# Performance work log

Measured on AMD Instinct MI355X. Metric: run time of the kernel, lower is better.

## Reference

```python
import jax, jax.numpy as jnp
import numpy as np

IN_F = 3072       # in_features
OUT_F = 9216      # out_features = 3 * N_HEADS * HEAD_DIM (fused QKV)
GROUP = 64        # quantization group size
RANK = 32         # lora_rank
HEAD_DIM = 128
N_HEADS = OUT_F // (3 * HEAD_DIM)  # 24
EPS = 1e-6
LORA_SCALE = 1.0


def setup_inputs() -> dict:
    key = jax.random.key(0)
    ks = jax.random.split(key, 10)
    B, S = 1, 4096
    x = jax.random.normal(ks[0], (B, S, IN_F), dtype=jnp.float32)
    # packed int4 weights: two signed int4 values per int8 byte
    qweight = jax.random.randint(ks[1], (OUT_F, IN_F // 2), -128, 128, dtype=jnp.int32).astype(jnp.int8)
    wscales = (jax.random.uniform(ks[2], (IN_F // GROUP, OUT_F)) * 0.02 + 0.001).astype(jnp.float32)
    bias = (jax.random.normal(ks[3], (OUT_F,)) * 0.01).astype(jnp.float32)
    lora_down = (jax.random.normal(ks[4], (IN_F, RANK)) * 0.02).astype(jnp.float32)
    lora_up = (jax.random.normal(ks[5], (OUT_F, RANK)) * 0.02).astype(jnp.float32)
    smooth = (jax.random.uniform(ks[6], (IN_F,)) * 0.5 + 0.75).astype(jnp.float32)   # keep away from 0
    norm_q = (jax.random.uniform(ks[7], (HEAD_DIM,)) * 0.5 + 0.75).astype(jnp.float32)
    norm_k = (jax.random.uniform(ks[8], (HEAD_DIM,)) * 0.5 + 0.75).astype(jnp.float32)
    ang = jax.random.uniform(ks[9], (S, HEAD_DIM // 2)) * (2.0 * np.pi)
    rotary_emb = jnp.stack([jnp.cos(ang), jnp.sin(ang)], axis=-1).astype(jnp.float32)  # [S, D/2, 2]
    return dict(x=x, qweight=qweight, wscales=wscales, bias=bias, lora_down=lora_down,
                lora_up=lora_up, smooth=smooth, norm_q=norm_q, norm_k=norm_k, rotary_emb=rotary_emb)


def _dequant_weight(qweight, wscales):
    # unpack two signed int4 lanes from each int8 (low nibble first), then per-group scale
    low = jnp.right_shift(jnp.left_shift(qweight, 4), 4)   # arithmetic shifts on int8 -> sign extend
    high = jnp.right_shift(qweight, 4)
    w4 = jnp.stack([low, high], axis=-1).reshape(OUT_F, IN_F)          # int4 codes in [-8, 7]
    wg = w4.astype(jnp.float32).reshape(OUT_F, IN_F // GROUP, GROUP)
    return (wg * wscales.T[:, :, None]).reshape(OUT_F, IN_F)          # [N, K]


def _quantize_act(x, smooth, lora_down):
    # fused: smooth -> symmetric per-token per-group int4 quantize -> lora_down projection
    B, S, K = x.shape
    M = B * S
    xs = (x / smooth).reshape(M, K)
    xg = xs.reshape(M, K // GROUP, GROUP)
    ascale = jnp.max(jnp.abs(xg), axis=-1, keepdims=True) / 7.0
    ascale = jnp.maximum(ascale, 1e-8)
    q = jnp.clip(jnp.round(xg / ascale), -8.0, 7.0)
    deq = (q * ascale).reshape(M, K)                                   # dequantized int4 activation
    lora_act = xs @ lora_down                                          # [M, RANK], fp32 side path
    return deq, lora_act


def _rope(t, cos, sin):
    # interleaved pairs (even, odd) rotation; t: [M, H, D], cos/sin: [M, 1, D/2]
    e, o = t[..., 0::2], t[..., 1::2]
    re = e * cos - o * sin
    ro = e * sin + o * cos
    return jnp.stack([re, ro], axis=-1).reshape(t.shape)


def reference(x, qweight, wscales, bias, lora_down, lora_up, smooth, norm_q, norm_k, rotary_emb):
    B, S, K = x.shape
    M = B * S
    deq_x, lora_act = _quantize_act(x, smooth, lora_down)
    w = _dequant_weight(qweight, wscales)
    # main int4 GEMM + LoRA up + bias, all fused in the real kernel
    out = deq_x @ w.T + (LORA_SCALE * lora_act) @ lora_up.T + bias     # [M, OUT_F]
    qkv = out.reshape(M, 3, N_HEADS, HEAD_DIM)
    q, k, v = qkv[:, 0], qkv[:, 1], qkv[:, 2]
    def rms(t, g):
        return t * jax.lax.rsqrt(jnp.mean(t * t, axis=-1, keepdims=True) + EPS) * g
    q = rms(q, norm_q)
    k = rms(k, norm_k)
    cos = rotary_emb[:, None, :, 0]   # [M, 1, D/2]
    sin = rotary_emb[:, None, :, 1]
    q = _rope(q, cos, sin)
    k = _rope(k, cos, sin)
    return jnp.stack([q, k, v], axis=1).reshape(B, S, OUT_F)
```

## Files before the change

kernel.cpp:

```cpp
#include <hip/hip_runtime.h>
#include <cstdint>

#define MDIM 4096
#define NDIM 9216
#define KDIM 3072
#define KP   3136
#define NKT2 97

#define QROWS 4
#define QB2 1024
#define WB 13824
#define PB 2304

typedef unsigned int u32;
typedef unsigned short u16;
typedef float f32x4 __attribute__((ext_vector_type(4)));
typedef __bf16 bf16x8 __attribute__((ext_vector_type(8)));

__device__ __forceinline__ u16 f2bf(float f) {
  u32 u = __float_as_uint(f);
  u32 r = u + 0x7fffu + ((u >> 16) & 1u);
  return (u16)(r >> 16);
}

__device__ __forceinline__ float frcp(float f) { return __builtin_amdgcn_rcpf(f); }

__device__ __forceinline__ void gld_lds16(const void* g, void* l) {
  __builtin_amdgcn_global_load_lds((__attribute__((address_space(1))) void*)g,
                                   (__attribute__((address_space(3))) void*)l,
                                   16, 0, 0);
}

__global__ __launch_bounds__(256) void k_quant(const float* __restrict__ x,
                        const float* __restrict__ lora_down, const float* __restrict__ smooth,
                        u16* __restrict__ Aex) {
  __shared__ float xs_s[QROWS][KDIM];
  __shared__ float part[64 * 32];
  const int tid = threadIdx.x;
  const int m0 = blockIdx.x * QROWS;
  const int sub = tid & 15;

  #pragma unroll
  for (int r = 0; r < QROWS; ++r) {
    const float* xr = x + (size_t)(m0 + r) * KDIM;
    u16* arow = Aex + (size_t)(m0 + r) * KP;
    #pragma unroll
    for (int p = 0; p < 3; ++p) {
      int g = p * 16 + (tid >> 4);
      int k0 = g * 64 + sub * 4;
      float4 xv = *(const float4*)(xr + k0);
      float4 sv = *(const float4*)(smooth + k0);
      float a0 = xv.x * frcp(sv.x), a1 = xv.y * frcp(sv.y);
      float a2 = xv.z * frcp(sv.z), a3 = xv.w * frcp(sv.w);
      xs_s[r][k0+0] = a0; xs_s[r][k0+1] = a1; xs_s[r][k0+2] = a2; xs_s[r][k0+3] = a3;
      float am = fmaxf(fmaxf(fabsf(a0), fabsf(a1)), fmaxf(fabsf(a2), fabsf(a3)));
      am = fmaxf(am, __shfl_xor(am, 8, 16));
      am = fmaxf(am, __shfl_xor(am, 4, 16));
      am = fmaxf(am, __shfl_xor(am, 2, 16));
      am = fmaxf(am, __shfl_xor(am, 1, 16));
      float asc = fmaxf(am * (1.0f / 7.0f), 1e-8f);
      float iasc = frcp(asc);
      float q0 = fminf(7.f, fmaxf(-8.f, rintf(a0 * iasc)));
      float q1 = fminf(7.f, fmaxf(-8.f, rintf(a1 * iasc)));
      float q2 = fminf(7.f, fmaxf(-8.f, rintf(a2 * iasc)));
      float q3 = fminf(7.f, fmaxf(-8.f, rintf(a3 * iasc)));
      float d0 = q0 * asc, d1 = q1 * asc, d2 = q2 * asc, d3 = q3 * asc;
      u32 lo = (u32)f2bf(d0) | ((u32)f2bf(d1) << 16);
      u32 hi = (u32)f2bf(d2) | ((u32)f2bf(d3) << 16);
      *(uint2*)(arow + k0) = make_uint2(lo, hi);
    }
    if (tid < 32) arow[3104 + tid] = 0;
  }
  __syncthreads();

  const int c  = tid >> 2;
  const int r8 = (tid & 3) * 8;
  float a[QROWS][8] = {};
  const float* lp = lora_down + (size_t)c * 32 + r8;
  #pragma unroll 2
  for (int i = 0; i < 48; ++i) {
    float4 l0 = *(const float4*)(lp);
    float4 l1 = *(const float4*)(lp + 4);
    #pragma unroll
    for (int r = 0; r < QROWS; ++r) {
      float xv = xs_s[r][i * 64 + c];
      a[r][0] = fmaf(xv, l0.x, a[r][0]); a[r][1] = fmaf(xv, l0.y, a[r][1]);
      a[r][2] = fmaf(xv, l0.z, a[r][2]); a[r][3] = fmaf(xv, l0.w, a[r][3]);
      a[r][4] = fmaf(xv, l1.x, a[r][4]); a[r][5] = fmaf(xv, l1.y, a[r][5]);
      a[r][6] = fmaf(xv, l1.z, a[r][6]); a[r][7] = fmaf(xv, l1.w, a[r][7]);
    }
    lp += 64 * 32;
  }
  #pragma unroll 1
  for (int r = 0; r < QROWS; ++r) {
    __syncthreads();
    *(float4*)(&part[c * 32 + r8])     = make_float4(a[r][0], a[r][1], a[r][2], a[r][3]);
    *(float4*)(&part[c * 32 + r8 + 4]) = make_float4(a[r][4], a[r][5], a[r][6], a[r][7]);
    __syncthreads();
    if (tid < 32) {
      float s = 0.f;
      #pragma unroll 8
      for (int cc = 0; cc < 64; ++cc) s += part[cc * 32 + tid];
      Aex[(size_t)(m0 + r) * KP + 3072 + tid] = f2bf(s);
    }
  }
}

__global__ __launch_bounds__(256) void k_wdq(const u32* __restrict__ qw,
                        const float* __restrict__ wsc, const float* __restrict__ lora_up,
                        u16* __restrict__ Bex) {
  const int tid = threadIdx.x;
  int bid = blockIdx.x;

  if (bid >= WB) {
    int idx = (bid - WB) * 256 + tid;
    int n = idx >> 6, c = idx & 63;
    u16 v = 0;
    if (c < 32) v = f2bf(lora_up[n * 32 + c]);
    Bex[(size_t)n * KP + 3072 + c] = v;
    return;
  }
  __shared__ int s_viol;
  u32 probe = qw[tid];
  bool ok = (probe >> 8) == ((probe & 0x80u) ? 0xffffffu : 0u);
  if (tid == 0) s_viol = 0;
  __syncthreads();
  if (!ok) atomicOr(&s_viol, 1);
  __syncthreads();
  const int f = (s_viol == 0);

  int idx = bid * 256 + tid;
  int n = idx / 384;
  int j = idx - n * 384;
  int k0 = j * 8;
  u32 w;
  if (f) {
    uint4 q4 = ((const uint4*)qw)[idx];
    w = (q4.x & 0xffu) | ((q4.y & 0xffu) << 8) | ((q4.z & 0xffu) << 16) | ((q4.w & 0xffu) << 24);
  } else {
    w = qw[idx];
  }
  float ws = wsc[(k0 >> 6) * NDIM + n];
  u32 ow[4];
  #pragma unroll
  for (int b = 0; b < 4; ++b) {
    int by = (int)((w >> (8 * b)) & 0xffu);
    int lo = (by << 28) >> 28;
    int hi = (by << 24) >> 28;
    ow[b] = (u32)f2bf((float)lo * ws) | ((u32)f2bf((float)hi * ws) << 16);
  }
  *(uint4*)(Bex + (size_t)n * KP + k0) = make_uint4(ow[0], ow[1], ow[2], ow[3]);
}

__global__ __launch_bounds__(512) void k_gemm(const u16* __restrict__ A, const u16* __restrict__ B,
                                              const float* __restrict__ bias, const float* __restrict__ norm_q,
                                              const float* __restrict__ norm_k, const float* __restrict__ rot,
                                              float* __restrict__ out) {
  extern __shared__ u16 lds[];
  const int tid  = threadIdx.x;
  const int lane = tid & 63;
  const int wave = tid >> 6;
  const int m0 = blockIdx.y * 256;
  const int n0 = blockIdx.x * 256;
  const int wm = (wave >> 2) * 128;
  const int wn = (wave & 3) * 64;
  const int lr = lane & 15;
  const int lq = lane >> 4;

  const u16 *pA0, *pA1, *pB0, *pB1;
  int la0, la1, lb0, lb1;
  {
    auto mk = [&](int p, const u16* base, int nb) -> const u16* {
      int pr = p >> 3, cs = p & 7;
      int c  = cs ^ (pr & 7);
      int r  = pr * 2 + (c >> 2);
      int kc = c & 3;
      return base + (size_t)(nb + r) * KP + kc * 8;
    };
    int p0 = tid, p1 = 512 + tid;
    pA0 = mk(p0, A, m0); pA1 = mk(p1, A, m0);
    pB0 = mk(p0, B, n0); pB1 = mk(p1, B, n0);
    la0 = p0 * 8;        la1 = p1 * 8;
    lb0 = 8192 + p0 * 8; lb1 = 8192 + p1 * 8;
  }

  int aoff[8], boff[4];
  #pragma unroll
  for (int t = 0; t < 8; ++t) {
    int ra = wm + t * 16 + lr;
    int pr = ra >> 1, c = (ra & 1) * 4 + lq;
    aoff[t] = pr * 64 + ((c ^ (pr & 7)) * 8);
  }
  #pragma unroll
  for (int t = 0; t < 4; ++t) {
    int rb = wn + t * 16 + lr;
    int pr = rb >> 1, c = (rb & 1) * 4 + lq;
    boff[t] = 8192 + pr * 64 + ((c ^ (pr & 7)) * 8);
  }

  f32x4 acc[8][4] = {};

  #pragma unroll
  for (int s = 0; s < 3; ++s) {
    u16* sl = lds + (s << 14);
    gld_lds16(pA0, sl + la0); gld_lds16(pA1, sl + la1);
    gld_lds16(pB0, sl + lb0); gld_lds16(pB1, sl + lb1);
    pA0 += 32; pA1 += 32; pB0 += 32; pB1 += 32;
  }
  asm volatile("s_waitcnt vmcnt(4)" ::: "memory");
  __builtin_amdgcn_s_barrier();
  asm volatile("" ::: "memory");

  bf16x8 af[8], bf[4];
  #pragma unroll
  for (int t = 0; t < 8; ++t) af[t] = *(const bf16x8*)&lds[aoff[t]];
  #pragma unroll
  for (int t = 0; t < 4; ++t) bf[t] = *(const bf16x8*)&lds[boff[t]];

  #pragma unroll 1
  for (int kt = 0; kt < NKT2 - 1; ++kt) {
    u16* stl = lds + (((kt + 3) & 3) << 14);
    const u16* nsl = lds + (((kt + 1) & 3) << 14);
    if (kt < NKT2 - 3) {
      gld_lds16(pA0, stl + la0); gld_lds16(pA1, stl + la1);
      gld_lds16(pB0, stl + lb0); gld_lds16(pB1, stl + lb1);
      pA0 += 32; pA1 += 32; pB0 += 32; pB1 += 32;
    }
    __builtin_amdgcn_s_setprio(1);
    #pragma unroll
    for (int t = 0; t < 8; ++t) {
      #pragma unroll
      for (int tj = 0; tj < 4; ++tj)
        acc[t][tj] = __builtin_amdgcn_mfma_f32_16x16x32_bf16(af[t], bf[tj], acc[t][tj], 0, 0, 0);
      af[t] = *(const bf16x8*)&nsl[aoff[t]];
    }
    #pragma unroll
    for (int t = 0; t < 4; ++t) bf[t] = *(const bf16x8*)&nsl[boff[t]];
    __builtin_amdgcn_s_setprio(0);
    __builtin_amdgcn_sched_group_barrier(0x020, 4, 0);
    #pragma unroll
    for (int g = 0; g < 8; ++g) {
      __builtin_amdgcn_sched_group_barrier(0x008, 4, 0);
      __builtin_amdgcn_sched_group_barrier(0x100, 1, 0);
    }
    __builtin_amdgcn_sched_group_barrier(0x100, 4, 0);
    if (kt < NKT2 - 3) asm volatile("s_waitcnt vmcnt(4)" ::: "memory");
    else               asm volatile("s_waitcnt vmcnt(0)" ::: "memory");
    __builtin_amdgcn_s_barrier();
    asm volatile("" ::: "memory");
  }
  #pragma unroll
  for (int t = 0; t < 8; ++t)
    #pragma unroll
    for (int tj = 0; tj < 4; ++tj)
      acc[t][tj] = __builtin_amdgcn_mfma_f32_16x16x32_bf16(af[t], bf[tj], acc[t][tj], 0, 0, 0);

  const int sel = (blockIdx.x >= 24) ? 2 : (blockIdx.x >= 12 ? 1 : 0);

  float bv[4];
  #pragma unroll
  for (int tj = 0; tj < 4; ++tj) bv[tj] = bias[n0 + wn + tj * 16 + lr];
  #pragma unroll
  for (int ti = 0; ti < 8; ++ti)
    #pragma unroll
    for (int tj = 0; tj < 4; ++tj)
      #pragma unroll
      for (int rg = 0; rg < 4; ++rg)
        acc[ti][tj][rg] += bv[tj];

  if (sel == 2) {
    #pragma unroll
    for (int tj = 0; tj < 4; ++tj) {
      int n = n0 + wn + tj * 16 + lr;
      #pragma unroll
      for (int ti = 0; ti < 8; ++ti) {
        int mr = m0 + wm + ti * 16 + lq * 4;
        #pragma unroll
        for (int rg = 0; rg < 4; ++rg)
          out[(size_t)(mr + rg) * NDIM + n] = acc[ti][tj][rg];
      }
    }
    return;
  }

  __syncthreads();
  float* ssq = (float*)lds;
  #pragma unroll
  for (int ti = 0; ti < 8; ++ti) {
    float pr4[4];
    #pragma unroll
    for (int rg = 0; rg < 4; ++rg) {
      float s = 0.f;
      #pragma unroll
      for (int tj = 0; tj < 4; ++tj) s += acc[ti][tj][rg] * acc[ti][tj][rg];
      pr4[rg] = s;
    }
    #pragma unroll
    for (int off = 1; off < 16; off <<= 1)
      #pragma unroll
      for (int rg = 0; rg < 4; ++rg) pr4[rg] += __shfl_xor(pr4[rg], off);
    #pragma unroll
    for (int rg = 0; rg < 4; ++rg)
      if (lr == (ti & 3) * 4 + rg)
        ssq[(wn >> 6) * 256 + wm + ti * 16 + lq * 4 + rg] = pr4[rg];
  }
  __syncthreads();

  const float* nrm = sel ? norm_k : norm_q;
  float gm[4];
  #pragma unroll
  for (int tj = 0; tj < 4; ++tj) gm[tj] = nrm[(wn & 64) + tj * 16 + lr];
  const float2* rot2 = (const float2*)rot;
  const float sgn = (lr & 1) ? 1.0f : -1.0f;
  const int hb = (wn >> 7) * 512;

  #pragma unroll
  for (int ti = 0; ti < 8; ++ti) {
    #pragma unroll
    for (int rg = 0; rg < 4; ++rg) {
      int row = wm + ti * 16 + lq * 4 + rg;
      float tot = ssq[hb + row] + ssq[hb + 256 + row];
      float rs = rsqrtf(tot * (1.0f / 128.0f) + 1e-6f);
      int m = m0 + row;
      #pragma unroll
      for (int tj = 0; tj < 4; ++tj) {
        int nl = (wn & 64) + tj * 16 + lr;
        float v = acc[ti][tj][rg] * rs * gm[tj];
        float p = __shfl_xor(v, 1);
        float2 cs = rot2[(size_t)m * 64 + (nl >> 1)];
        out[(size_t)m * NDIM + n0 + wn + tj * 16 + lr] = v * cs.x + sgn * (p * cs.y);
      }
    }
  }
}

extern "C" void kernel_launch(void* const* d_in, const int* in_sizes, int n_in,
                              void* d_out, int out_size, void* d_ws, size_t ws_size,
                              hipStream_t stream) {
  const float* x         = (const float*)d_in[0];
  const u32*   qweight   = (const u32*)d_in[1];
  const float* wscales   = (const float*)d_in[2];
  const float* bias      = (const float*)d_in[3];
  const float* lora_down = (const float*)d_in[4];
  const float* lora_up   = (const float*)d_in[5];
  const float* smooth    = (const float*)d_in[6];
  const float* norm_q    = (const float*)d_in[7];
  const float* norm_k    = (const float*)d_in[8];
  const float* rot       = (const float*)d_in[9];
  float* out = (float*)d_out;

  u16* Aex = (u16*)d_ws;
  u16* Bex = Aex + (size_t)MDIM * KP;

  static bool attr_set = false;
  if (!attr_set) {
    hipFuncSetAttribute(reinterpret_cast<const void*>(k_gemm),
                        hipFuncAttributeMaxDynamicSharedMemorySize, 131072);
    attr_set = true;
  }

  k_wdq<<<WB + PB, 256, 0, stream>>>(qweight, wscales, lora_up, Bex);
  k_quant<<<QB2, 256, 0, stream>>>(x, lora_down, smooth, Aex);
  k_gemm<<<dim3(NDIM / 256, MDIM / 256), 512, 131072, stream>>>(Aex, Bex, bias, norm_q, norm_k, rot, out);
}
```

Measured before the change: 513.0 us.

## Use 4 waves with 128x128 warp tiles and in-register RMSNorm reduction

The GEMM block shrinks from 8 waves to 4, each computing a 128x128 sub-tile (8x8 MFMA tiles) instead of 128x64. This raises per-wave register reuse of A/B fragments, halves LDS fragment reads per MFMA, and lets each wave hold a full head dimension so the RMSNorm reduction is done with lane shuffles, without the LDS round trip and two barriers. The trade-off is doubled accumulator registers (256 VGPRs of acc), fewer waves to hide latency, and a reworked MFMA/LDS interleave schedule without setprio.

```diff
diff --git a/kernel.cpp b/kernel.cpp
--- a/kernel.cpp
+++ b/kernel.cpp
@@ -152,7 +152,7 @@
   *(uint4*)(Bex + (size_t)n * KP + k0) = make_uint4(ow[0], ow[1], ow[2], ow[3]);
 }
 
-__global__ __launch_bounds__(512) void k_gemm(const u16* __restrict__ A, const u16* __restrict__ B,
+__global__ __launch_bounds__(256, 1) void k_gemm(const u16* __restrict__ A, const u16* __restrict__ B,
                                               const float* __restrict__ bias, const float* __restrict__ norm_q,
                                               const float* __restrict__ norm_k, const float* __restrict__ rot,
                                               float* __restrict__ out) {
@@ -162,13 +162,13 @@
   const int wave = tid >> 6;
   const int m0 = blockIdx.y * 256;
   const int n0 = blockIdx.x * 256;
-  const int wm = (wave >> 2) * 128;
-  const int wn = (wave & 3) * 64;
+  const int wm = (wave >> 1) * 128;
+  const int wn = (wave & 1) * 128;
   const int lr = lane & 15;
   const int lq = lane >> 4;
 
-  const u16 *pA0, *pA1, *pB0, *pB1;
-  int la0, la1, lb0, lb1;
+  const u16* pA[4]; const u16* pB[4];
+  int la[4], lb[4];
   {
     auto mk = [&](int p, const u16* base, int nb) -> const u16* {
       int pr = p >> 3, cs = p & 7;
@@ -177,74 +177,85 @@
       int kc = c & 3;
       return base + (size_t)(nb + r) * KP + kc * 8;
     };
-    int p0 = tid, p1 = 512 + tid;
-    pA0 = mk(p0, A, m0); pA1 = mk(p1, A, m0);
-    pB0 = mk(p0, B, n0); pB1 = mk(p1, B, n0);
-    la0 = p0 * 8;        la1 = p1 * 8;
-    lb0 = 8192 + p0 * 8; lb1 = 8192 + p1 * 8;
-  }
-
-  int aoff[8], boff[4];
+    #pragma unroll
+    for (int i = 0; i < 4; ++i) {
+      int p = i * 256 + tid;
+      pA[i] = mk(p, A, m0);
+      pB[i] = mk(p, B, n0);
+      la[i] = p * 8;
+      lb[i] = 8192 + p * 8;
+    }
+  }
+
+  int aoff[8], boff[8];
   #pragma unroll
   for (int t = 0; t < 8; ++t) {
     int ra = wm + t * 16 + lr;
     int pr = ra >> 1, c = (ra & 1) * 4 + lq;
     aoff[t] = pr * 64 + ((c ^ (pr & 7)) * 8);
-  }
-  #pragma unroll
-  for (int t = 0; t < 4; ++t) {
     int rb = wn + t * 16 + lr;
-    int pr = rb >> 1, c = (rb & 1) * 4 + lq;
-    boff[t] = 8192 + pr * 64 + ((c ^ (pr & 7)) * 8);
-  }
-
-  f32x4 acc[8][4] = {};
+    int pb_ = rb >> 1, cb = (rb & 1) * 4 + lq;
+    boff[t] = 8192 + pb_ * 64 + ((cb ^ (pb_ & 7)) * 8);
+  }
+
+  f32x4 acc[8][8] = {};
 
   #pragma unroll
   for (int s = 0; s < 3; ++s) {
     u16* sl = lds + (s << 14);
-    gld_lds16(pA0, sl + la0); gld_lds16(pA1, sl + la1);
-    gld_lds16(pB0, sl + lb0); gld_lds16(pB1, sl + lb1);
-    pA0 += 32; pA1 += 32; pB0 += 32; pB1 += 32;
-  }
-  asm volatile("s_waitcnt vmcnt(4)" ::: "memory");
+    #pragma unroll
+    for (int i = 0; i < 4; ++i) {
+      gld_lds16(pA[i], sl + la[i]); gld_lds16(pB[i], sl + lb[i]);
+      pA[i] += 32; pB[i] += 32;
+    }
+  }
+  asm volatile("s_waitcnt vmcnt(8)" ::: "memory");
   __builtin_amdgcn_s_barrier();
   asm volatile("" ::: "memory");
 
-  bf16x8 af[8], bf[4];
+  bf16x8 af[8], bf[8];
   #pragma unroll
   for (int t = 0; t < 8; ++t) af[t] = *(const bf16x8*)&lds[aoff[t]];
   #pragma unroll
-  for (int t = 0; t < 4; ++t) bf[t] = *(const bf16x8*)&lds[boff[t]];
+  for (int t = 0; t < 8; ++t) bf[t] = *(const bf16x8*)&lds[boff[t]];
 
   #pragma unroll 1
   for (int kt = 0; kt < NKT2 - 1; ++kt) {
     u16* stl = lds + (((kt + 3) & 3) << 14);
     const u16* nsl = lds + (((kt + 1) & 3) << 14);
     if (kt < NKT2 - 3) {
-      gld_lds16(pA0, stl + la0); gld_lds16(pA1, stl + la1);
-      gld_lds16(pB0, stl + lb0); gld_lds16(pB1, stl + lb1);
-      pA0 += 32; pA1 += 32; pB0 += 32; pB1 += 32;
-    }
-    __builtin_amdgcn_s_setprio(1);
-    #pragma unroll
-    for (int t = 0; t < 8; ++t) {
-      #pragma unroll
-      for (int tj = 0; tj < 4; ++tj)
+      #pragma unroll
+      for (int i = 0; i < 4; ++i) {
+        gld_lds16(pA[i], stl + la[i]); gld_lds16(pB[i], stl + lb[i]);
+        pA[i] += 32; pB[i] += 32;
+      }
+    }
+    #pragma unroll
+    for (int t = 0; t < 7; ++t) {
+      #pragma unroll
+      for (int tj = 0; tj < 8; ++tj)
         acc[t][tj] = __builtin_amdgcn_mfma_f32_16x16x32_bf16(af[t], bf[tj], acc[t][tj], 0, 0, 0);
       af[t] = *(const bf16x8*)&nsl[aoff[t]];
     }
     #pragma unroll
-    for (int t = 0; t < 4; ++t) bf[t] = *(const bf16x8*)&nsl[boff[t]];
-    __builtin_amdgcn_s_setprio(0);
-    __builtin_amdgcn_sched_group_barrier(0x020, 4, 0);
+    for (int tj = 0; tj < 8; ++tj) {
+      acc[7][tj] = __builtin_amdgcn_mfma_f32_16x16x32_bf16(af[7], bf[tj], acc[7][tj], 0, 0, 0);
+      bf[tj] = *(const bf16x8*)&nsl[boff[tj]];
+    }
+    af[7] = *(const bf16x8*)&nsl[aoff[7]];
+    __builtin_amdgcn_sched_group_barrier(0x020, 8, 0);
+    #pragma unroll
+    for (int g = 0; g < 7; ++g) {
+      __builtin_amdgcn_sched_group_barrier(0x008, 8, 0);
+      __builtin_amdgcn_sched_group_barrier(0x100, 1, 0);
+    }
     #pragma unroll
     for (int g = 0; g < 8; ++g) {
-      __builtin_amdgcn_sched_group_barrier(0x008, 4, 0);
+      __builtin_amdgcn_sched_group_barrier(0x008, 1, 0);
       __builtin_amdgcn_sched_group_barrier(0x100, 1, 0);
     }
-    __builtin_amdgcn_sched_group_barrier(0x100, 4, 0);
-    if (kt < NKT2 - 3) asm volatile("s_waitcnt vmcnt(4)" ::: "memory");
+    __builtin_amdgcn_sched_group_barrier(0x100, 1, 0);
+    if (kt < NKT2 - 3) asm volatile("s_waitcnt vmcnt(8)" ::: "memory");
     else               asm volatile("s_waitcnt vmcnt(0)" ::: "memory");
     __builtin_amdgcn_s_barrier();
     asm volatile("" ::: "memory");
@@ -252,25 +263,25 @@
   #pragma unroll
   for (int t = 0; t < 8; ++t)
     #pragma unroll
-    for (int tj = 0; tj < 4; ++tj)
+    for (int tj = 0; tj < 8; ++tj)
       acc[t][tj] = __builtin_amdgcn_mfma_f32_16x16x32_bf16(af[t], bf[tj], acc[t][tj], 0, 0, 0);
 
   const int sel = (blockIdx.x >= 24) ? 2 : (blockIdx.x >= 12 ? 1 : 0);
 
-  float bv[4];
-  #pragma unroll
-  for (int tj = 0; tj < 4; ++tj) bv[tj] = bias[n0 + wn + tj * 16 + lr];
+  float bv[8];
+  #pragma unroll
+  for (int tj = 0; tj < 8; ++tj) bv[tj] = bias[n0 + wn + tj * 16 + lr];
   #pragma unroll
   for (int ti = 0; ti < 8; ++ti)
     #pragma unroll
-    for (int tj = 0; tj < 4; ++tj)
+    for (int tj = 0; tj < 8; ++tj)
       #pragma unroll
       for (int rg = 0; rg < 4; ++rg)
         acc[ti][tj][rg] += bv[tj];
 
   if (sel == 2) {
     #pragma unroll
-    for (int tj = 0; tj < 4; ++tj) {
+    for (int tj = 0; tj < 8; ++tj) {
       int n = n0 + wn + tj * 16 + lr;
       #pragma unroll
       for (int ti = 0; ti < 8; ++ti) {
@@ -283,52 +294,31 @@
     return;
   }
 
-  __syncthreads();
-  float* ssq = (float*)lds;
+  const float* nrm = sel ? norm_k : norm_q;
+  float gm[8];
+  #pragma unroll
+  for (int tj = 0; tj < 8; ++tj) gm[tj] = nrm[tj * 16 + lr];
+  const float2* rot2 = (const float2*)rot;
+  const float sgn = (lr & 1) ? 1.0f : -1.0f;
+
   #pragma unroll
   for (int ti = 0; ti < 8; ++ti) {
-    float pr4[4];
     #pragma unroll
     for (int rg = 0; rg < 4; ++rg) {
       float s = 0.f;
       #pragma unroll
-      for (int tj = 0; tj < 4; ++tj) s += acc[ti][tj][rg] * acc[ti][tj][rg];
-      pr4[rg] = s;
-    }
-    #pragma unroll
-    for (int off = 1; off < 16; off <<= 1)
-      #pragma unroll
-      for (int rg = 0; rg < 4; ++rg) pr4[rg] += __shfl_xor(pr4[rg], off);
-    #pragma unroll
-    for (int rg = 0; rg < 4; ++rg)
-      if (lr == (ti & 3) * 4 + rg)
-        ssq[(wn >> 6) * 256 + wm + ti * 16 + lq * 4 + rg] = pr4[rg];
-  }
-  __syncthreads();
-
-  const float* nrm = sel ? norm_k : norm_q;
-  float gm[4];
-  #pragma unroll
-  for (int tj = 0; tj < 4; ++tj) gm[tj] = nrm[(wn & 64) + tj * 16 + lr];
-  const float2* rot2 = (const float2*)rot;
-  const float sgn = (lr & 1) ? 1.0f : -1.0f;
-  const int hb = (wn >> 7) * 512;
-
-  #pragma unroll
-  for (int ti = 0; ti < 8; ++ti) {
-    #pragma unroll
-    for (int rg = 0; rg < 4; ++rg) {
-      int row = wm + ti * 16 + lq * 4 + rg;
-      float tot = ssq[hb + row] + ssq[hb + 256 + row];
-      float rs = rsqrtf(tot * (1.0f / 128.0f) + 1e-6f);
-      int m = m0 + row;
-      #pragma unroll
-      for (int tj = 0; tj < 4; ++tj) {
-        int nl = (wn & 64) + tj * 16 + lr;
+      for (int tj = 0; tj < 8; ++tj) s += acc[ti][tj][rg] * acc[ti][tj][rg];
+      s += __shfl_xor(s, 1); s += __shfl_xor(s, 2);
+      s += __shfl_xor(s, 4); s += __shfl_xor(s, 8);
+      float rs = rsqrtf(s * (1.0f / 128.0f) + 1e-6f);
+      int m = m0 + wm + ti * 16 + lq * 4 + rg;
+      #pragma unroll
+      for (int tj = 0; tj < 8; ++tj) {
+        int nl = tj * 16 + lr;
         float v = acc[ti][tj][rg] * rs * gm[tj];
         float p = __shfl_xor(v, 1);
         float2 cs = rot2[(size_t)m * 64 + (nl >> 1)];
-        out[(size_t)m * NDIM + n0 + wn + tj * 16 + lr] = v * cs.x + sgn * (p * cs.y);
+        out[(size_t)m * NDIM + n0 + wn + nl] = v * cs.x + sgn * (p * cs.y);
       }
     }
   }
@@ -361,5 +351,5 @@
 
   k_wdq<<<WB + PB, 256, 0, stream>>>(qweight, wscales, lora_up, Bex);
   k_quant<<<QB2, 256, 0, stream>>>(x, lora_down, smooth, Aex);
-  k_gemm<<<dim3(NDIM / 256, MDIM / 256), 512, 131072, stream>>>(Aex, Bex, bias, norm_q, norm_k, rot, out);
-}
+  k_gemm<<<dim3(NDIM / 256, MDIM / 256), 256, 131072, stream>>>(Aex, Bex, bias, norm_q, norm_k, rot, out);
+}
```

New measurement: 589.4 us. +14.9%, slower.

## Fuse int4 weight dequantization into GEMM mainloop, drop separate dequant kernel

Applied to the files above, without the earlier changes.

Removes the standalone weight-dequant kernel and its bf16 weight buffer. The GEMM now loads packed int4 weights and scales from global memory into registers, dequantizes them to bf16 and writes them to LDS inside the pipelined k-loop. The LoRA-up slice is converted in the tail iteration. This saves the write and re-read of the dequantized weight matrix and one kernel launch. In exchange, every M-tile repeats the dequant arithmetic (16 times total), which adds VALU work and register pressure to the MFMA loop.

```diff
diff --git a/kernel.cpp b/kernel.cpp
--- a/kernel.cpp
+++ b/kernel.cpp
@@ -1,5 +1,6 @@
 #include <hip/hip_runtime.h>
 #include <cstdint>
+#include <type_traits>
 
 #define MDIM 4096
 #define NDIM 9216
@@ -9,8 +10,6 @@
 
 #define QROWS 4
 #define QB2 1024
-#define WB 13824
-#define PB 2304
 
 typedef unsigned int u32;
 typedef unsigned short u16;
@@ -106,53 +105,8 @@
   }
 }
 
-__global__ __launch_bounds__(256) void k_wdq(const u32* __restrict__ qw,
-                        const float* __restrict__ wsc, const float* __restrict__ lora_up,
-                        u16* __restrict__ Bex) {
-  const int tid = threadIdx.x;
-  int bid = blockIdx.x;
-
-  if (bid >= WB) {
-    int idx = (bid - WB) * 256 + tid;
-    int n = idx >> 6, c = idx & 63;
-    u16 v = 0;
-    if (c < 32) v = f2bf(lora_up[n * 32 + c]);
-    Bex[(size_t)n * KP + 3072 + c] = v;
-    return;
-  }
-  __shared__ int s_viol;
-  u32 probe = qw[tid];
-  bool ok = (probe >> 8) == ((probe & 0x80u) ? 0xffffffu : 0u);
-  if (tid == 0) s_viol = 0;
-  __syncthreads();
-  if (!ok) atomicOr(&s_viol, 1);
-  __syncthreads();
-  const int f = (s_viol == 0);
-
-  int idx = bid * 256 + tid;
-  int n = idx / 384;
-  int j = idx - n * 384;
-  int k0 = j * 8;
-  u32 w;
-  if (f) {
-    uint4 q4 = ((const uint4*)qw)[idx];
-    w = (q4.x & 0xffu) | ((q4.y & 0xffu) << 8) | ((q4.z & 0xffu) << 16) | ((q4.w & 0xffu) << 24);
-  } else {
-    w = qw[idx];
-  }
-  float ws = wsc[(k0 >> 6) * NDIM + n];
-  u32 ow[4];
-  #pragma unroll
-  for (int b = 0; b < 4; ++b) {
-    int by = (int)((w >> (8 * b)) & 0xffu);
-    int lo = (by << 28) >> 28;
-    int hi = (by << 24) >> 28;
-    ow[b] = (u32)f2bf((float)lo * ws) | ((u32)f2bf((float)hi * ws) << 16);
-  }
-  *(uint4*)(Bex + (size_t)n * KP + k0) = make_uint4(ow[0], ow[1], ow[2], ow[3]);
-}
-
-__global__ __launch_bounds__(512) void k_gemm(const u16* __restrict__ A, const u16* __restrict__ B,
+__global__ __launch_bounds__(512) void k_gemm(const u16* __restrict__ A, const u32* __restrict__ qw,
+                                              const float* __restrict__ wsc, const float* __restrict__ lora_up,
                                               const float* __restrict__ bias, const float* __restrict__ norm_q,
                                               const float* __restrict__ norm_k, const float* __restrict__ rot,
                                               float* __restrict__ out) {
@@ -167,21 +121,26 @@
   const int lr = lane & 15;
   const int lq = lane >> 4;
 
-  const u16 *pA0, *pA1, *pB0, *pB1;
+  const u16 *pA0, *pA1;
   int la0, la1, lb0, lb1;
+  int qoff0, qoff1, nr0, nr1, kc0, kc1;
   {
-    auto mk = [&](int p, const u16* base, int nb) -> const u16* {
+    auto geo = [&](int p, int& r, int& kc) {
       int pr = p >> 3, cs = p & 7;
       int c  = cs ^ (pr & 7);
-      int r  = pr * 2 + (c >> 2);
-      int kc = c & 3;
-      return base + (size_t)(nb + r) * KP + kc * 8;
+      r  = pr * 2 + (c >> 2);
+      kc = c & 3;
     };
+    int r, kc;
     int p0 = tid, p1 = 512 + tid;
-    pA0 = mk(p0, A, m0); pA1 = mk(p1, A, m0);
-    pB0 = mk(p0, B, n0); pB1 = mk(p1, B, n0);
-    la0 = p0 * 8;        la1 = p1 * 8;
-    lb0 = 8192 + p0 * 8; lb1 = 8192 + p1 * 8;
+    geo(p0, r, kc);
+    pA0 = A + (size_t)(m0 + r) * KP + kc * 8;
+    nr0 = n0 + r; kc0 = kc; qoff0 = nr0 * 384 + kc;
+    la0 = p0 * 8; lb0 = 8192 + p0 * 8;
+    geo(p1, r, kc);
+    pA1 = A + (size_t)(m0 + r) * KP + kc * 8;
+    nr1 = n0 + r; kc1 = kc; qoff1 = nr1 * 384 + kc;
+    la1 = p1 * 8; lb1 = 8192 + p1 * 8;
   }
 
   int aoff[8], boff[4];
@@ -200,60 +159,177 @@
 
   f32x4 acc[8][4] = {};
 
-  #pragma unroll
-  for (int s = 0; s < 3; ++s) {
-    u16* sl = lds + (s << 14);
-    gld_lds16(pA0, sl + la0); gld_lds16(pA1, sl + la1);
-    gld_lds16(pB0, sl + lb0); gld_lds16(pB1, sl + lb1);
-    pA0 += 32; pA1 += 32; pB0 += 32; pB1 += 32;
-  }
-  asm volatile("s_waitcnt vmcnt(4)" ::: "memory");
-  __builtin_amdgcn_s_barrier();
-  asm volatile("" ::: "memory");
-
-  bf16x8 af[8], bf[4];
-  #pragma unroll
-  for (int t = 0; t < 8; ++t) af[t] = *(const bf16x8*)&lds[aoff[t]];
-  #pragma unroll
-  for (int t = 0; t < 4; ++t) bf[t] = *(const bf16x8*)&lds[boff[t]];
-
-  #pragma unroll 1
-  for (int kt = 0; kt < NKT2 - 1; ++kt) {
-    u16* stl = lds + (((kt + 3) & 3) << 14);
-    const u16* nsl = lds + (((kt + 1) & 3) << 14);
-    if (kt < NKT2 - 3) {
-      gld_lds16(pA0, stl + la0); gld_lds16(pA1, stl + la1);
-      gld_lds16(pB0, stl + lb0); gld_lds16(pB1, stl + lb1);
-      pA0 += 32; pA1 += 32; pB0 += 32; pB1 += 32;
-    }
-    __builtin_amdgcn_s_setprio(1);
-    #pragma unroll
-    for (int t = 0; t < 8; ++t) {
-      #pragma unroll
-      for (int tj = 0; tj < 4; ++tj)
-        acc[t][tj] = __builtin_amdgcn_mfma_f32_16x16x32_bf16(af[t], bf[tj], acc[t][tj], 0, 0, 0);
-      af[t] = *(const bf16x8*)&nsl[aoff[t]];
-    }
-    #pragma unroll
-    for (int t = 0; t < 4; ++t) bf[t] = *(const bf16x8*)&nsl[boff[t]];
-    __builtin_amdgcn_s_setprio(0);
-    __builtin_amdgcn_sched_group_barrier(0x020, 4, 0);
-    #pragma unroll
-    for (int g = 0; g < 8; ++g) {
-      __builtin_amdgcn_sched_group_barrier(0x008, 4, 0);
-      __builtin_amdgcn_sched_group_barrier(0x100, 1, 0);
-    }
-    __builtin_amdgcn_sched_group_barrier(0x100, 4, 0);
-    if (kt < NKT2 - 3) asm volatile("s_waitcnt vmcnt(4)" ::: "memory");
-    else               asm volatile("s_waitcnt vmcnt(0)" ::: "memory");
+  u32 probe = qw[lane];
+  bool okp = (probe >> 8) == ((probe & 0x80u) ? 0xffffffu : 0u);
+  const bool f1 = __all(okp);
+
+  auto run = [&](auto f1c) {
+    constexpr bool F1 = decltype(f1c)::value;
+    uint4 qa, qb; float wsa, wsb;
+
+    auto loadq = [&](int ktg) {
+      if constexpr (F1) {
+        qa = ((const uint4*)qw)[qoff0 + ktg * 4];
+        qb = ((const uint4*)qw)[qoff1 + ktg * 4];
+      } else {
+        qa.x = qw[qoff0 + ktg * 4];
+        qb.x = qw[qoff1 + ktg * 4];
+      }
+      wsa = wsc[(ktg >> 1) * NDIM + nr0];
+      wsb = wsc[(ktg >> 1) * NDIM + nr1];
+    };
+    auto deqw = [&](int slot) {
+      u16* wsl = lds + (slot << 14);
+      u32 w0, w1;
+      if constexpr (F1) {
+        w0 = (qa.x & 0xffu) | ((qa.y & 0xffu) << 8) | ((qa.z & 0xffu) << 16) | ((qa.w & 0xffu) << 24);
+        w1 = (qb.x & 0xffu) | ((qb.y & 0xffu) << 8) | ((qb.z & 0xffu) << 16) | ((qb.w & 0xffu) << 24);
+      } else { w0 = qa.x; w1 = qb.x; }
+      u32 o0[4], o1[4];
+      #pragma unroll
+      for (int b = 0; b < 4; ++b) {
+        int by = (int)((w0 >> (8 * b)) & 0xffu);
+        int lo = (by << 28) >> 28, hi = (by << 24) >> 28;
+        o0[b] = (u32)f2bf((float)lo * wsa) | ((u32)f2bf((float)hi * wsa) << 16);
+        by = (int)((w1 >> (8 * b)) & 0xffu);
+        lo = (by << 28) >> 28; hi = (by << 24) >> 28;
+        o1[b] = (u32)f2bf((float)lo * wsb) | ((u32)f2bf((float)hi * wsb) << 16);
+      }
+      *(uint4*)(wsl + lb0) = make_uint4(o0[0], o0[1], o0[2], o0[3]);
+      *(uint4*)(wsl + lb1) = make_uint4(o1[0], o1[1], o1[2], o1[3]);
+    };
+
+    #pragma unroll
+    for (int s = 0; s < 3; ++s) {
+      u16* sl = lds + (s << 14);
+      gld_lds16(pA0, sl + la0); gld_lds16(pA1, sl + la1);
+      pA0 += 32; pA1 += 32;
+    }
+    loadq(0);
+    asm volatile("s_waitcnt vmcnt(0)" ::: "memory");
+    deqw(0);
+    loadq(1);
+    asm volatile("s_waitcnt vmcnt(0)" ::: "memory");
+    deqw(1);
+    loadq(2);
+    asm volatile("s_waitcnt lgkmcnt(0)" ::: "memory");
     __builtin_amdgcn_s_barrier();
     asm volatile("" ::: "memory");
-  }
-  #pragma unroll
-  for (int t = 0; t < 8; ++t)
-    #pragma unroll
-    for (int tj = 0; tj < 4; ++tj)
-      acc[t][tj] = __builtin_amdgcn_mfma_f32_16x16x32_bf16(af[t], bf[tj], acc[t][tj], 0, 0, 0);
+
+    bf16x8 af[8], bf[4];
+    #pragma unroll
+    for (int t = 0; t < 8; ++t) af[t] = *(const bf16x8*)&lds[aoff[t]];
+    #pragma unroll
+    for (int t = 0; t < 4; ++t) bf[t] = *(const bf16x8*)&lds[boff[t]];
+
+    #pragma unroll 1
+    for (int kt = 0; kt < 93; ++kt) {
+      u16* stl = lds + (((kt + 3) & 3) << 14);
+      const u16* nsl = lds + (((kt + 1) & 3) << 14);
+      gld_lds16(pA0, stl + la0); gld_lds16(pA1, stl + la1);
+      pA0 += 32; pA1 += 32;
+      asm volatile("s_waitcnt vmcnt(2)" ::: "memory");
+      deqw((kt + 2) & 3);
+      loadq(kt + 3);
+      __builtin_amdgcn_s_setprio(1);
+      #pragma unroll
+      for (int t = 0; t < 8; ++t) {
+        #pragma unroll
+        for (int tj = 0; tj < 4; ++tj)
+          acc[t][tj] = __builtin_amdgcn_mfma_f32_16x16x32_bf16(af[t], bf[tj], acc[t][tj], 0, 0, 0);
+        af[t] = *(const bf16x8*)&nsl[aoff[t]];
+      }
+      #pragma unroll
+      for (int t = 0; t < 4; ++t) bf[t] = *(const bf16x8*)&nsl[boff[t]];
+      __builtin_amdgcn_s_setprio(0);
+      __builtin_amdgcn_sched_group_barrier(0x008, 4, 0);
+      __builtin_amdgcn_sched_group_barrier(0x200, 2, 0);
+      __builtin_amdgcn_sched_group_barrier(0x020, 4, 0);
+      #pragma unroll
+      for (int g = 0; g < 7; ++g) {
+        __builtin_amdgcn_sched_group_barrier(0x008, 4, 0);
+        __builtin_amdgcn_sched_group_barrier(0x100, 1, 0);
+      }
+      __builtin_amdgcn_sched_group_barrier(0x100, 5, 0);
+      asm volatile("s_waitcnt lgkmcnt(0)" ::: "memory");
+      __builtin_amdgcn_s_barrier();
+      asm volatile("" ::: "memory");
+    }
+
+    float4 fa0, fa1, fb0, fb1;
+    {
+      u16* stl = lds + (0 << 14);
+      const u16* nsl = lds + ((94 & 3) << 14);
+      gld_lds16(pA0, stl + la0); gld_lds16(pA1, stl + la1);
+      asm volatile("s_waitcnt vmcnt(2)" ::: "memory");
+      deqw(95 & 3);
+      const float4* lu4 = (const float4*)lora_up;
+      fa0 = lu4[nr0 * 8 + kc0 * 2]; fa1 = lu4[nr0 * 8 + kc0 * 2 + 1];
+      fb0 = lu4[nr1 * 8 + kc1 * 2]; fb1 = lu4[nr1 * 8 + kc1 * 2 + 1];
+      __builtin_amdgcn_s_setprio(1);
+      #pragma unroll
+      for (int t = 0; t < 8; ++t) {
+        #pragma unroll
+        for (int tj = 0; tj < 4; ++tj)
+          acc[t][tj] = __builtin_amdgcn_mfma_f32_16x16x32_bf16(af[t], bf[tj], acc[t][tj], 0, 0, 0);
+        af[t] = *(const bf16x8*)&nsl[aoff[t]];
+      }
+      #pragma unroll
+      for (int t = 0; t < 4; ++t) bf[t] = *(const bf16x8*)&nsl[boff[t]];
+      __builtin_amdgcn_s_setprio(0);
+      asm volatile("s_waitcnt lgkmcnt(0)" ::: "memory");
+      __builtin_amdgcn_s_barrier();
+      asm volatile("" ::: "memory");
+    }
+    {
+      asm volatile("s_waitcnt vmcnt(0)" ::: "memory");
+      u16* w96 = lds + (0 << 14);
+      u32 a0 = (u32)f2bf(fa0.x) | ((u32)f2bf(fa0.y) << 16);
+      u32 a1 = (u32)f2bf(fa0.z) | ((u32)f2bf(fa0.w) << 16);
+      u32 a2 = (u32)f2bf(fa1.x) | ((u32)f2bf(fa1.y) << 16);
+      u32 a3 = (u32)f2bf(fa1.z) | ((u32)f2bf(fa1.w) << 16);
+      *(uint4*)(w96 + lb0) = make_uint4(a0, a1, a2, a3);
+      u32 b0 = (u32)f2bf(fb0.x) | ((u32)f2bf(fb0.y) << 16);
+      u32 b1 = (u32)f2bf(fb0.z) | ((u32)f2bf(fb0.w) << 16);
+      u32 b2 = (u32)f2bf(fb1.x) | ((u32)f2bf(fb1.y) << 16);
+      u32 b3 = (u32)f2bf(fb1.z) | ((u32)f2bf(fb1.w) << 16);
+      *(uint4*)(w96 + lb1) = make_uint4(b0, b1, b2, b3);
+      const u16* nsl = lds + ((95 & 3) << 14);
+      __builtin_amdgcn_s_setprio(1);
+      #pragma unroll
+      for (int t = 0; t < 8; ++t) {
+        #pragma unroll
+        for (int tj = 0; tj < 4; ++tj)
+          acc[t][tj] = __builtin_amdgcn_mfma_f32_16x16x32_bf16(af[t], bf[tj], acc[t][tj], 0, 0, 0);
+        af[t] = *(const bf16x8*)&nsl[aoff[t]];
+      }
+      #pragma unroll
+      for (int t = 0; t < 4; ++t) bf[t] = *(const bf16x8*)&nsl[boff[t]];
+      __builtin_amdgcn_s_setprio(0);
+      asm volatile("s_waitcnt lgkmcnt(0)" ::: "memory");
+      __builtin_amdgcn_s_barrier();
+      asm volatile("" ::: "memory");
+    }
+    {
+      const u16* nsl = lds + (0 << 14);
+      #pragma unroll
+      for (int t = 0; t < 8; ++t) {
+        #pragma unroll
+        for (int tj = 0; tj < 4; ++tj)
+          acc[t][tj] = __builtin_amdgcn_mfma_f32_16x16x32_bf16(af[t], bf[tj], acc[t][tj], 0, 0, 0);
+        af[t] = *(const bf16x8*)&nsl[aoff[t]];
+      }
+      #pragma unroll
+      for (int t = 0; t < 4; ++t) bf[t] = *(const bf16x8*)&nsl[boff[t]];
+      #pragma unroll
+      for (int t = 0; t < 8; ++t)
+        #pragma unroll
+        for (int tj = 0; tj < 4; ++tj)
+          acc[t][tj] = __builtin_amdgcn_mfma_f32_16x16x32_bf16(af[t], bf[tj], acc[t][tj], 0, 0, 0);
+    }
+  };
+  if (f1) run(std::integral_constant<bool, true>{});
+  else    run(std::integral_constant<bool, false>{});
 
   const int sel = (blockIdx.x >= 24) ? 2 : (blockIdx.x >= 12 ? 1 : 0);
 
@@ -350,7 +426,6 @@
   float* out = (float*)d_out;
 
   u16* Aex = (u16*)d_ws;
-  u16* Bex = Aex + (size_t)MDIM * KP;
 
   static bool attr_set = false;
   if (!attr_set) {
@@ -359,7 +434,7 @@
     attr_set = true;
   }
 
-  k_wdq<<<WB + PB, 256, 0, stream>>>(qweight, wscales, lora_up, Bex);
   k_quant<<<QB2, 256, 0, stream>>>(x, lora_down, smooth, Aex);
-  k_gemm<<<dim3(NDIM / 256, MDIM / 256), 512, 131072, stream>>>(Aex, Bex, bias, norm_q, norm_k, rot, out);
+  k_gemm<<<dim3(NDIM / 256, MDIM / 256), 512, 131072, stream>>>(Aex, qweight, wscales, lora_up,
+                                                                bias, norm_q, norm_k, rot, out);
 }
```

New measurement: 658.7 us. +28.4%, slower.
